# Optimization experiments

Measured on AMD Instinct MI355X. Metric: run time of the kernel, lower is better.

The kernel has to match this reference:

```python
import jax, jax.numpy as jnp
import numpy as np

B, D, E, H, OUT = 4096, 1024, 8, 4096, 1024


def setup_inputs() -> dict:
    key = jax.random.key(0)
    ks = jax.random.split(key, 8)
    s_in = 1.0 / np.sqrt(D)
    s_h = 1.0 / np.sqrt(H)
    return {
        "x": jax.random.normal(ks[0], (B, D), dtype=jnp.float32),
        "Wg": jax.random.uniform(ks[1], (D, E), minval=-s_in, maxval=s_in, dtype=jnp.float32),
        "bg": jnp.zeros((E,), dtype=jnp.float32),
        "W1": jax.random.uniform(ks[2], (E, D, H), minval=-s_in, maxval=s_in, dtype=jnp.float32),
        "b1": jnp.zeros((E, H), dtype=jnp.float32),
        "W2": jax.random.uniform(ks[3], (E, H, OUT), minval=-s_h, maxval=s_h, dtype=jnp.float32),
        "b2": jnp.zeros((E, OUT), dtype=jnp.float32),
        "w_bal": jnp.float32(0.01),
    }


def reference(x, Wg, bg, W1, b1, W2, b2, w_bal):
    # Gating: softmax then top-1 (== argmax of logits)
    gate_logits = x @ Wg + bg                      # [B, E]
    assign = jnp.argmax(gate_logits, axis=1)       # [B] top-1 expert
    onehot = jax.nn.one_hot(assign, E, dtype=x.dtype)  # [B, E] dispatch mask

    # Dense dispatch: run every expert MLP, combine by one-hot (top-1 select).
    # Original returns raw expert output (no gate-prob scaling).
    h = jax.nn.relu(jnp.einsum("bd,edh->ebh", x, W1) + b1[:, None, :])  # [E, B, H]
    y = jnp.einsum("ebh,eho->ebo", h, W2) + b2[:, None, :]              # [E, B, OUT]
    output = jnp.einsum("ebo,be->bo", y, onehot)                        # [B, OUT]

    # Load-balance loss on per-expert token counts
    loads = onehot.sum(axis=0)                     # [E]
    balance_loss = jnp.sum((loads - loads.mean()) ** 2) / E
    return output, balance_loss * w_bal
```

## Files before the change

### kernel.cpp

```cpp
#include <hip/hip_runtime.h>
#include <hip/hip_bf16.h>

typedef unsigned short u16;
typedef __attribute__((ext_vector_type(8))) short bf16x8;
typedef __attribute__((ext_vector_type(8))) unsigned short u16x8;
typedef __attribute__((ext_vector_type(4))) float f32x4;

#define BTOK 4096
#define DDIM 1024
#define NEXP 8
#define HDIM 4096
#define ODIM 1024
#define HC 2048
#define MAXTILES 40
#define MAXROWS (MAXTILES * 128)

__device__ __forceinline__ u16 f2bf(float f) {
  unsigned u = __float_as_uint(f);
  return (u16)((u + 0x7FFFu + ((u >> 16) & 1u)) >> 16);
}
__device__ __forceinline__ float bf2f(u16 v) {
  return __uint_as_float(((unsigned)v) << 16);
}

__device__ __forceinline__ void gload16(const void* g, void* l) {
  __builtin_amdgcn_global_load_lds(
      (const __attribute__((address_space(1))) void*)g,
      (__attribute__((address_space(3))) void*)l, 16, 0, 0);
}

__global__ __launch_bounds__(256) void gate_kernel(
    const float* __restrict__ x, const float* __restrict__ Wg,
    const float* __restrict__ bg, int* __restrict__ assign,
    int* __restrict__ counts) {
  int wave = threadIdx.x >> 6;
  int lane = threadIdx.x & 63;
  int b = blockIdx.x * 4 + wave;
  const float* xr = x + (size_t)b * DDIM;
  double acc[NEXP];
#pragma unroll
  for (int e = 0; e < NEXP; ++e) acc[e] = 0.0;
  for (int d = lane; d < DDIM; d += 64) {
    float xv = xr[d];
    const float4* wrow = (const float4*)(Wg + d * NEXP);
    float4 w0 = wrow[0], w1 = wrow[1];
    acc[0] += (double)xv * (double)w0.x;
    acc[1] += (double)xv * (double)w0.y;
    acc[2] += (double)xv * (double)w0.z;
    acc[3] += (double)xv * (double)w0.w;
    acc[4] += (double)xv * (double)w1.x;
    acc[5] += (double)xv * (double)w1.y;
    acc[6] += (double)xv * (double)w1.z;
    acc[7] += (double)xv * (double)w1.w;
  }
#pragma unroll
  for (int e = 0; e < NEXP; ++e) {
    double v = acc[e];
#pragma unroll
    for (int off = 32; off > 0; off >>= 1) v += __shfl_xor(v, off);
    acc[e] = v;
  }
  if (lane == 0) {
    int best = 0;
    double bv = acc[0] + (double)bg[0];
#pragma unroll
    for (int e = 1; e < NEXP; ++e) {
      double v = acc[e] + (double)bg[e];
      if (v > bv) { bv = v; best = e; }
    }
    assign[b] = best;
    atomicAdd(&counts[best], 1);
  }
}

__global__ void setup_kernel(const int* __restrict__ counts,
                             const float* __restrict__ wbal,
                             int* __restrict__ offp, int* __restrict__ tile_e,
                             int* __restrict__ tile_m, int* __restrict__ meta,
                             float* __restrict__ loss_out) {
  if (threadIdx.x != 0 || blockIdx.x != 0) return;
  int off = 0, nt = 0;
  for (int e = 0; e < NEXP; ++e) {
    offp[e] = off;
    int pc = (counts[e] + 127) & ~127;
    for (int t = 0; t < (pc >> 7); ++t) {
      tile_e[nt] = e;
      tile_m[nt] = off + t * 128;
      ++nt;
    }
    off += pc;
  }
  offp[NEXP] = off;
  meta[0] = nt;
  float mean = (float)BTOK / (float)NEXP;
  float s = 0.f;
  for (int e = 0; e < NEXP; ++e) {
    float d = (float)counts[e] - mean;
    s += d * d;
  }
  loss_out[0] = s / (float)NEXP * wbal[0];
}

__global__ __launch_bounds__(256) void gather_kernel(
    const float* __restrict__ x, const int* __restrict__ assign,
    const int* __restrict__ offp, int* __restrict__ fill,
    int* __restrict__ rowmap, u16* __restrict__ xg) {
  int b = blockIdx.x;
  __shared__ int srow;
  if (threadIdx.x == 0) {
    int e = assign[b];
    int pos = atomicAdd(&fill[e], 1);
    int row = offp[e] + pos;
    rowmap[row] = b;
    srow = row;
  }
  __syncthreads();
  int row = srow;
  float4 v = *(const float4*)(x + (size_t)b * DDIM + threadIdx.x * 4);
  ushort4 o;
  o.x = f2bf(v.x);
  o.y = f2bf(v.y);
  o.z = f2bf(v.z);
  o.w = f2bf(v.w);
  *(ushort4*)(xg + (size_t)row * DDIM + threadIdx.x * 4) = o;
}

__global__ __launch_bounds__(256) void transpose_conv(
    const float* __restrict__ W, u16* __restrict__ wt, int inN,
    size_t estrideIn, int k0, int n0, int KR, int NC) {
  const int e = blockIdx.z;
  const int kb = blockIdx.x * 64, nb = blockIdx.y * 64;
  __shared__ float lds[64][68];
  const float* src = W + (size_t)e * estrideIn + (size_t)k0 * inN + n0;
  const int t = threadIdx.x;
  const int rr = t >> 4, cc = (t & 15) * 4;
#pragma unroll
  for (int p = 0; p < 4; ++p) {
    float4 v = *(const float4*)(src + (size_t)(kb + rr + p * 16) * inN + nb + cc);
    *(float4*)&lds[rr + p * 16][cc] = v;
  }
  __syncthreads();
  const int n = t >> 2, kg = (t & 3) * 16;
  u16 tmp[16];
#pragma unroll
  for (int i = 0; i < 16; ++i) tmp[i] = f2bf(lds[kg + i][n]);
  u16* dst = wt + ((size_t)e * NC + nb + n) * KR + kb + kg;
  *(float4*)dst = *(float4*)&tmp[0];
  *(float4*)(dst + 8) = *(float4*)&tmp[8];
}

template <int MODE>
__global__ __launch_bounds__(256) void moe_gemm(
    const u16* __restrict__ A, int lda, const u16* __restrict__ BT, int ldb,
    int nbRows, const float* __restrict__ bias, int biasLd, int cOff,
    const int* __restrict__ tile_e, const int* __restrict__ tile_m,
    const int* __restrict__ meta, u16* __restrict__ Hout, int ldh,
    u16* __restrict__ P, size_t pStride) {
  const int nx = gridDim.x;
  const int nwg = nx * gridDim.y;
  const int orig = blockIdx.y * nx + blockIdx.x;
  const int q = nwg >> 3;
  const int wg = (orig & 7) * q + (orig >> 3);
  const int bx = wg % nx, by = wg / nx;
  if (bx >= meta[0]) return;
  const int e = tile_e[bx];
  const int m0 = tile_m[bx];
  const int n0 = by * 128;
  const int kOff = blockIdx.z << 10;

  __shared__ __align__(16) u16 lds[2 * 8192];

  const int tid = threadIdx.x;
  const int lane = tid & 63;
  const int wave = tid >> 6;
  const int wr = wave >> 1, wc = wave & 1;
  const int fr = lane & 15;
  const int kqr = lane >> 4;

  const int r0 = tid >> 2, k0 = (tid & 3) ^ ((r0 >> 1) & 3);
  const int r1 = (tid + 256) >> 2, k1 = ((tid + 256) & 3) ^ ((r1 >> 1) & 3);
  const u16* aS0 = A + (size_t)(m0 + r0) * lda + kOff + k0 * 8;
  const u16* aS1 = A + (size_t)(m0 + r1) * lda + kOff + k1 * 8;
  const u16* bPan = BT + ((size_t)e * nbRows + n0) * ldb + kOff;
  const u16* bS0 = bPan + (size_t)r0 * ldb + k0 * 8;
  const u16* bS1 = bPan + (size_t)r1 * ldb + k1 * 8;
  const int dst0 = (tid & ~63) * 8;
  const int dst1 = dst0 + 2048;

  int aOff[4], bOff[4];
#pragma unroll
  for (int i = 0; i < 4; ++i) {
    int r = wr * 64 + i * 16 + fr;
    aOff[i] = (r * 4 + (kqr ^ ((r >> 1) & 3))) * 8;
    int c = wc * 64 + i * 16 + fr;
    bOff[i] = (c * 4 + (kqr ^ ((c >> 1) & 3))) * 8;
  }

  f32x4 acc[4][4];
#pragma unroll
  for (int i = 0; i < 4; ++i)
#pragma unroll
    for (int j = 0; j < 4; ++j)
#pragma unroll
      for (int r = 0; r < 4; ++r) acc[i][j][r] = 0.f;

  auto stage = [&](int c, int kt) {
    const int ko = kt * 32;
    u16* base = lds + c * 8192;
    gload16(aS0 + ko, base + dst0);
    gload16(aS1 + ko, base + dst1);
    gload16(bS0 + ko, base + 4096 + dst0);
    gload16(bS1 + ko, base + 4096 + dst1);
  };
  auto compute = [&](int c) {
    const u16* base = lds + c * 8192;
    bf16x8 af[4], bfr[4];
#pragma unroll
    for (int i = 0; i < 4; ++i) {
      af[i] = *(const bf16x8*)(base + aOff[i]);
      bfr[i] = *(const bf16x8*)(base + 4096 + bOff[i]);
    }
#pragma unroll
    for (int i = 0; i < 4; ++i)
#pragma unroll
      for (int j = 0; j < 4; ++j)
        acc[i][j] = __builtin_amdgcn_mfma_f32_16x16x32_bf16(af[i], bfr[j],
                                                            acc[i][j], 0, 0, 0);
  };

  stage(0, 0);
  __syncthreads();
  int cur = 0;
#pragma unroll 1
  for (int kt = 0; kt < 31; ++kt) {
    stage(cur ^ 1, kt + 1);
    compute(cur);
    __syncthreads();
    cur ^= 1;
  }
  compute(cur);

  if constexpr (MODE == 0) {
#pragma unroll
    for (int i = 0; i < 4; ++i) {
      int rbase = m0 + wr * 64 + i * 16 + (lane >> 4) * 4;
#pragma unroll
      for (int j = 0; j < 4; ++j) {
        int col = n0 + wc * 64 + j * 16 + fr;
        float bv = bias[e * biasLd + cOff + col];
#pragma unroll
        for (int r = 0; r < 4; ++r) {
          float v = acc[i][j][r] + bv;
          v = v > 0.f ? v : 0.f;
          Hout[(size_t)(rbase + r) * ldh + col] = f2bf(v);
        }
      }
    }
  } else {
    u16* Pp = P + blockIdx.z * pStride;
#pragma unroll
    for (int i = 0; i < 4; ++i) {
      int rbase = m0 + wr * 64 + i * 16 + (lane >> 4) * 4;
#pragma unroll
      for (int j = 0; j < 4; ++j) {
        int col = n0 + wc * 64 + j * 16 + fr;
#pragma unroll
        for (int r = 0; r < 4; ++r) {
          size_t idx = (size_t)(rbase + r) * ODIM + col;
          if constexpr (MODE == 1)
            Pp[idx] = f2bf(acc[i][j][r]);
          else
            Pp[idx] = f2bf(bf2f(Pp[idx]) + acc[i][j][r]);
        }
      }
    }
  }
}

__global__ __launch_bounds__(256) void reduce_kernel(
    const u16* __restrict__ P, size_t pStride, const int* __restrict__ rowmap,
    const int* __restrict__ tile_e, const int* __restrict__ tile_m,
    const int* __restrict__ meta, const float* __restrict__ b2,
    float* __restrict__ out) {
  if ((int)blockIdx.x >= meta[0]) return;
  const int e = tile_e[blockIdx.x];
  const int row = tile_m[blockIdx.x] + (threadIdx.x >> 1);
  const int tok = rowmap[row];
  if (tok < 0) return;
  const int c0 = blockIdx.y * 128 + (threadIdx.x & 1) * 64;
  const u16* p0 = P + (size_t)row * ODIM;
  const u16* p1 = p0 + pStride;
  float* o = out + (size_t)tok * ODIM;
#pragma unroll
  for (int j = 0; j < 8; ++j) {
    int c = c0 + j * 8;
    u16x8 a = *(const u16x8*)(p0 + c);
    u16x8 b = *(const u16x8*)(p1 + c);
    float4 v0, v1;
    v0.x = bf2f(a[0]) + bf2f(b[0]) + b2[e * ODIM + c + 0];
    v0.y = bf2f(a[1]) + bf2f(b[1]) + b2[e * ODIM + c + 1];
    v0.z = bf2f(a[2]) + bf2f(b[2]) + b2[e * ODIM + c + 2];
    v0.w = bf2f(a[3]) + bf2f(b[3]) + b2[e * ODIM + c + 3];
    v1.x = bf2f(a[4]) + bf2f(b[4]) + b2[e * ODIM + c + 4];
    v1.y = bf2f(a[5]) + bf2f(b[5]) + b2[e * ODIM + c + 5];
    v1.z = bf2f(a[6]) + bf2f(b[6]) + b2[e * ODIM + c + 6];
    v1.w = bf2f(a[7]) + bf2f(b[7]) + b2[e * ODIM + c + 7];
    *(float4*)(o + c) = v0;
    *(float4*)(o + c + 4) = v1;
  }
}

extern "C" void kernel_launch(void* const* d_in, const int* in_sizes, int n_in,
                              void* d_out, int out_size, void* d_ws,
                              size_t ws_size, hipStream_t stream) {
  const float* x = (const float*)d_in[0];
  const float* Wg = (const float*)d_in[1];
  const float* bg = (const float*)d_in[2];
  const float* W1 = (const float*)d_in[3];
  const float* b1 = (const float*)d_in[4];
  const float* W2 = (const float*)d_in[5];
  const float* b2 = (const float*)d_in[6];
  const float* wbal = (const float*)d_in[7];
  float* out = (float*)d_out;

  char* ws = (char*)d_ws;
  int* counts = (int*)(ws + 0);
  int* fill = (int*)(ws + 64);
  int* offp = (int*)(ws + 128);
  int* meta = (int*)(ws + 192);
  int* tile_e = (int*)(ws + 256);
  int* tile_m = (int*)(ws + 512);
  int* assign = (int*)(ws + 4096);
  int* rowmap = (int*)(ws + 20480);
  u16* xg = (u16*)(ws + 65536);
  u16* h = (u16*)(ws + 10551296);
  u16* wt = (u16*)(ws + 52494336);
  u16* P = (u16*)(ws + 86048768);
  const size_t hChunk = (size_t)MAXROWS * HC;
  const size_t pStride = (size_t)MAXROWS * ODIM;

  hipMemsetAsync(ws, 0, 4096, stream);
  hipMemsetAsync(rowmap, 0xFF, MAXROWS * 4, stream);
  hipMemsetAsync(xg, 0, (size_t)MAXROWS * DDIM * 2, stream);

  gate_kernel<<<BTOK / 4, 256, 0, stream>>>(x, Wg, bg, assign, counts);
  setup_kernel<<<1, 64, 0, stream>>>(counts, wbal, offp, tile_e, tile_m, meta,
                                     out + (size_t)BTOK * ODIM);
  gather_kernel<<<BTOK, 256, 0, stream>>>(x, assign, offp, fill, rowmap, xg);

  for (int c = 0; c < 2; ++c) {
    u16* hc = h + (size_t)c * hChunk;
    transpose_conv<<<dim3(DDIM / 64, HC / 64, NEXP), 256, 0, stream>>>(
        W1, wt, HDIM, (size_t)DDIM * HDIM, 0, c * HC, DDIM, HC);
    moe_gemm<0><<<dim3(MAXTILES, HC / 128, 1), 256, 0, stream>>>(
        xg, DDIM, wt, DDIM, HC, b1, HDIM, c * HC, tile_e, tile_m, meta, hc, HC,
        nullptr, 0);
    transpose_conv<<<dim3(HC / 64, ODIM / 64, NEXP), 256, 0, stream>>>(
        W2, wt, ODIM, (size_t)HDIM * ODIM, c * HC, 0, HC, ODIM);
    if (c == 0)
      moe_gemm<1><<<dim3(MAXTILES, ODIM / 128, 2), 256, 0, stream>>>(
          hc, HC, wt, HC, ODIM, nullptr, 0, 0, tile_e, tile_m, meta, nullptr, 0,
          P, pStride);
    else
      moe_gemm<2><<<dim3(MAXTILES, ODIM / 128, 2), 256, 0, stream>>>(
          hc, HC, wt, HC, ODIM, nullptr, 0, 0, tile_e, tile_m, meta, nullptr, 0,
          P, pStride);
  }
  reduce_kernel<<<dim3(MAXTILES, ODIM / 128), 256, 0, stream>>>(
      P, pStride, rowmap, tile_e, tile_m, meta, b2, out);
}
```

Before: 370.1 us.

## Adapt hidden chunk size to workspace, use fp32 partials, replace memsets

The hidden-dimension chunk size is now chosen from the workspace size, so a single chunk of 4096 can be used when space allows, with separate W1/W2 transposed buffers and a runtime k-tile count. Partial sums are kept in fp32 instead of bf16, the reduce kernel is restructured into coalesced float4 loops, and the transpose write mapping is changed. The three memsets are replaced by one init kernel, and the xg zeroing is dropped. Fewer chunks cut launch and K-split overhead. fp32 partials double the partial-buffer traffic but improve accuracy, and dropping the xg zeroing leaves padded rows holding stale data, whose outputs are discarded through rowmap.

```diff
diff --git a/kernel.cpp b/kernel.cpp
--- a/kernel.cpp
+++ b/kernel.cpp
@@ -3,7 +3,6 @@
 
 typedef unsigned short u16;
 typedef __attribute__((ext_vector_type(8))) short bf16x8;
-typedef __attribute__((ext_vector_type(8))) unsigned short u16x8;
 typedef __attribute__((ext_vector_type(4))) float f32x4;
 
 #define BTOK 4096
@@ -11,22 +10,27 @@
 #define NEXP 8
 #define HDIM 4096
 #define ODIM 1024
-#define HC 2048
 #define MAXTILES 40
 #define MAXROWS (MAXTILES * 128)
 
 __device__ __forceinline__ u16 f2bf(float f) {
   unsigned u = __float_as_uint(f);
   return (u16)((u + 0x7FFFu + ((u >> 16) & 1u)) >> 16);
-}
-__device__ __forceinline__ float bf2f(u16 v) {
-  return __uint_as_float(((unsigned)v) << 16);
 }
 
 __device__ __forceinline__ void gload16(const void* g, void* l) {
   __builtin_amdgcn_global_load_lds(
       (const __attribute__((address_space(1))) void*)g,
       (__attribute__((address_space(3))) void*)l, 16, 0, 0);
+}
+
+__global__ __launch_bounds__(256) void init_kernel(int* __restrict__ ctrl,
+                                                   int* __restrict__ rowmap) {
+  int i = blockIdx.x * 256 + threadIdx.x;
+  if (i < 1024)
+    ctrl[i] = 0;
+  else
+    rowmap[i - 1024] = -1;
 }
 
 __global__ __launch_bounds__(256) void gate_kernel(
@@ -140,7 +144,7 @@
     *(float4*)&lds[rr + p * 16][cc] = v;
   }
   __syncthreads();
-  const int n = t >> 2, kg = (t & 3) * 16;
+  const int n = t & 63, kg = (t >> 6) * 16;
   u16 tmp[16];
 #pragma unroll
   for (int i = 0; i < 16; ++i) tmp[i] = f2bf(lds[kg + i][n]);
@@ -155,7 +159,7 @@
     int nbRows, const float* __restrict__ bias, int biasLd, int cOff,
     const int* __restrict__ tile_e, const int* __restrict__ tile_m,
     const int* __restrict__ meta, u16* __restrict__ Hout, int ldh,
-    u16* __restrict__ P, size_t pStride) {
+    float* __restrict__ P, size_t pStride, int nkt) {
   const int nx = gridDim.x;
   const int nwg = nx * gridDim.y;
   const int orig = blockIdx.y * nx + blockIdx.x;
@@ -166,7 +170,7 @@
   const int e = tile_e[bx];
   const int m0 = tile_m[bx];
   const int n0 = by * 128;
-  const int kOff = blockIdx.z << 10;
+  const int kOff = blockIdx.z * nkt * 32;
 
   __shared__ __align__(16) u16 lds[2 * 8192];
 
@@ -232,7 +236,7 @@
   __syncthreads();
   int cur = 0;
 #pragma unroll 1
-  for (int kt = 0; kt < 31; ++kt) {
+  for (int kt = 0; kt < nkt - 1; ++kt) {
     stage(cur ^ 1, kt + 1);
     compute(cur);
     __syncthreads();
@@ -257,7 +261,7 @@
       }
     }
   } else {
-    u16* Pp = P + blockIdx.z * pStride;
+    float* Pp = P + blockIdx.z * pStride;
 #pragma unroll
     for (int i = 0; i < 4; ++i) {
       int rbase = m0 + wr * 64 + i * 16 + (lane >> 4) * 4;
@@ -268,9 +272,9 @@
         for (int r = 0; r < 4; ++r) {
           size_t idx = (size_t)(rbase + r) * ODIM + col;
           if constexpr (MODE == 1)
-            Pp[idx] = f2bf(acc[i][j][r]);
+            Pp[idx] = acc[i][j][r];
           else
-            Pp[idx] = f2bf(bf2f(Pp[idx]) + acc[i][j][r]);
+            Pp[idx] += acc[i][j][r];
         }
       }
     }
@@ -278,35 +282,31 @@
 }
 
 __global__ __launch_bounds__(256) void reduce_kernel(
-    const u16* __restrict__ P, size_t pStride, const int* __restrict__ rowmap,
+    const float* __restrict__ P, size_t pStride, const int* __restrict__ rowmap,
     const int* __restrict__ tile_e, const int* __restrict__ tile_m,
     const int* __restrict__ meta, const float* __restrict__ b2,
     float* __restrict__ out) {
   if ((int)blockIdx.x >= meta[0]) return;
   const int e = tile_e[blockIdx.x];
-  const int row = tile_m[blockIdx.x] + (threadIdx.x >> 1);
-  const int tok = rowmap[row];
-  if (tok < 0) return;
-  const int c0 = blockIdx.y * 128 + (threadIdx.x & 1) * 64;
-  const u16* p0 = P + (size_t)row * ODIM;
-  const u16* p1 = p0 + pStride;
-  float* o = out + (size_t)tok * ODIM;
-#pragma unroll
-  for (int j = 0; j < 8; ++j) {
-    int c = c0 + j * 8;
-    u16x8 a = *(const u16x8*)(p0 + c);
-    u16x8 b = *(const u16x8*)(p1 + c);
-    float4 v0, v1;
-    v0.x = bf2f(a[0]) + bf2f(b[0]) + b2[e * ODIM + c + 0];
-    v0.y = bf2f(a[1]) + bf2f(b[1]) + b2[e * ODIM + c + 1];
-    v0.z = bf2f(a[2]) + bf2f(b[2]) + b2[e * ODIM + c + 2];
-    v0.w = bf2f(a[3]) + bf2f(b[3]) + b2[e * ODIM + c + 3];
-    v1.x = bf2f(a[4]) + bf2f(b[4]) + b2[e * ODIM + c + 4];
-    v1.y = bf2f(a[5]) + bf2f(b[5]) + b2[e * ODIM + c + 5];
-    v1.z = bf2f(a[6]) + bf2f(b[6]) + b2[e * ODIM + c + 6];
-    v1.w = bf2f(a[7]) + bf2f(b[7]) + b2[e * ODIM + c + 7];
-    *(float4*)(o + c) = v0;
-    *(float4*)(o + c + 4) = v1;
+  const int m0 = tile_m[blockIdx.x];
+  const int c0 = blockIdx.y * 128;
+#pragma unroll 1
+  for (int it = 0; it < 16; ++it) {
+    int idx = it * 256 + threadIdx.x;
+    int r = idx >> 5, cq = idx & 31;
+    int row = m0 + r;
+    int tok = rowmap[row];
+    if (tok < 0) continue;
+    int c = c0 + cq * 4;
+    float4 a = *(const float4*)(P + (size_t)row * ODIM + c);
+    float4 b = *(const float4*)(P + pStride + (size_t)row * ODIM + c);
+    float4 bb = *(const float4*)(b2 + (size_t)e * ODIM + c);
+    float4 o;
+    o.x = a.x + b.x + bb.x;
+    o.y = a.y + b.y + bb.y;
+    o.z = a.z + b.z + bb.z;
+    o.w = a.w + b.w + bb.w;
+    *(float4*)(out + (size_t)tok * ODIM + c) = o;
   }
 }
 
@@ -333,38 +333,46 @@
   int* assign = (int*)(ws + 4096);
   int* rowmap = (int*)(ws + 20480);
   u16* xg = (u16*)(ws + 65536);
-  u16* h = (u16*)(ws + 10551296);
-  u16* wt = (u16*)(ws + 52494336);
-  u16* P = (u16*)(ws + 86048768);
-  const size_t hChunk = (size_t)MAXROWS * HC;
+
+  const size_t hOff = 65536 + (size_t)MAXROWS * DDIM * 2;
+  auto need = [&](size_t hc) {
+    return hOff + (size_t)MAXROWS * hc * 2
+           + (size_t)NEXP * hc * DDIM * 2
+           + (size_t)NEXP * ODIM * hc * 2
+           + 2 * (size_t)MAXROWS * ODIM * 4;
+  };
+  size_t HC = 4096;
+  if (ws_size < need(4096)) HC = (ws_size >= need(2048)) ? 2048 : 1024;
+
+  u16* h = (u16*)(ws + hOff);
+  u16* wt1 = (u16*)((char*)h + (size_t)MAXROWS * HC * 2);
+  u16* wt2 = (u16*)((char*)wt1 + (size_t)NEXP * HC * DDIM * 2);
+  float* P = (float*)((char*)wt2 + (size_t)NEXP * ODIM * HC * 2);
   const size_t pStride = (size_t)MAXROWS * ODIM;
 
-  hipMemsetAsync(ws, 0, 4096, stream);
-  hipMemsetAsync(rowmap, 0xFF, MAXROWS * 4, stream);
-  hipMemsetAsync(xg, 0, (size_t)MAXROWS * DDIM * 2, stream);
-
+  init_kernel<<<24, 256, 0, stream>>>((int*)ws, rowmap);
   gate_kernel<<<BTOK / 4, 256, 0, stream>>>(x, Wg, bg, assign, counts);
   setup_kernel<<<1, 64, 0, stream>>>(counts, wbal, offp, tile_e, tile_m, meta,
                                      out + (size_t)BTOK * ODIM);
   gather_kernel<<<BTOK, 256, 0, stream>>>(x, assign, offp, fill, rowmap, xg);
 
-  for (int c = 0; c < 2; ++c) {
-    u16* hc = h + (size_t)c * hChunk;
+  const int nch = HDIM / (int)HC;
+  for (int c = 0; c < nch; ++c) {
     transpose_conv<<<dim3(DDIM / 64, HC / 64, NEXP), 256, 0, stream>>>(
-        W1, wt, HDIM, (size_t)DDIM * HDIM, 0, c * HC, DDIM, HC);
+        W1, wt1, HDIM, (size_t)DDIM * HDIM, 0, c * (int)HC, DDIM, (int)HC);
     moe_gemm<0><<<dim3(MAXTILES, HC / 128, 1), 256, 0, stream>>>(
-        xg, DDIM, wt, DDIM, HC, b1, HDIM, c * HC, tile_e, tile_m, meta, hc, HC,
-        nullptr, 0);
+        xg, DDIM, wt1, DDIM, (int)HC, b1, HDIM, c * (int)HC, tile_e, tile_m,
+        meta, h, (int)HC, nullptr, 0, DDIM / 32);
     transpose_conv<<<dim3(HC / 64, ODIM / 64, NEXP), 256, 0, stream>>>(
-        W2, wt, ODIM, (size_t)HDIM * ODIM, c * HC, 0, HC, ODIM);
+        W2, wt2, ODIM, (size_t)HDIM * ODIM, c * (int)HC, 0, (int)HC, ODIM);
     if (c == 0)
       moe_gemm<1><<<dim3(MAXTILES, ODIM / 128, 2), 256, 0, stream>>>(
-          hc, HC, wt, HC, ODIM, nullptr, 0, 0, tile_e, tile_m, meta, nullptr, 0,
-          P, pStride);
+          h, (int)HC, wt2, (int)HC, ODIM, nullptr, 0, 0, tile_e, tile_m, meta,
+          nullptr, 0, P, pStride, (int)HC / 64);
     else
       moe_gemm<2><<<dim3(MAXTILES, ODIM / 128, 2), 256, 0, stream>>>(
-          hc, HC, wt, HC, ODIM, nullptr, 0, 0, tile_e, tile_m, meta, nullptr, 0,
-          P, pStride);
+          h, (int)HC, wt2, (int)HC, ODIM, nullptr, 0, 0, tile_e, tile_m, meta,
+          nullptr, 0, P, pStride, (int)HC / 64);
   }
   reduce_kernel<<<dim3(MAXTILES, ODIM / 128), 256, 0, stream>>>(
       P, pStride, rowmap, tile_e, tile_m, meta, b2, out);
```

Result: faster. 359.9 us (-2.7%).
